# Optimization experiments

Hardware: AMD Instinct MI355X
Metric: run time of the kernel (lower is better)

## Reference

```python
import jax, jax.numpy as jnp
import numpy as np

B, T, C, NH = 8, 1024, 768, 12
HD = C // NH


def setup_inputs() -> dict:
    key = jax.random.key(0)
    k1, k2, k3, k4, k5 = jax.random.split(key, 5)
    s = 0.02
    return {
        "x": jax.random.normal(k1, (B, T, C), dtype=jnp.float32),
        "w_attn": jax.random.normal(k2, (C, 3 * C), dtype=jnp.float32) * s,
        "b_attn": jax.random.normal(k3, (3 * C,), dtype=jnp.float32) * s,
        "w_proj": jax.random.normal(k4, (C, C), dtype=jnp.float32) * s,
        "b_proj": jax.random.normal(k5, (C,), dtype=jnp.float32) * s,
    }


def reference(x, w_attn, b_attn, w_proj, b_proj):
    Bv, Tv, Cv = x.shape
    # fused QKV projection
    qkv = jnp.einsum('btc,cd->btd', x, w_attn) + b_attn  # [B,T,3C]
    q, k, v = jnp.split(qkv, 3, axis=-1)
    # [B, NH, T, HD]
    q = q.reshape(Bv, Tv, NH, HD).transpose(0, 2, 1, 3)
    k = k.reshape(Bv, Tv, NH, HD).transpose(0, 2, 1, 3)
    v = v.reshape(Bv, Tv, NH, HD).transpose(0, 2, 1, 3)
    scale = 1.0 / np.sqrt(HD).astype(np.float32)
    att = jnp.einsum('bhqd,bhkd->bhqk', q, k) * scale  # [B,NH,T,T]
    causal = jnp.tril(jnp.ones((Tv, Tv), dtype=bool))
    att = jnp.where(causal, att, -jnp.inf)
    att = jax.nn.softmax(att, axis=-1)
    y = jnp.einsum('bhqk,bhkd->bhqd', att, v)  # [B,NH,T,HD]
    y = y.transpose(0, 2, 1, 3).reshape(Bv, Tv, Cv)
    return jnp.einsum('btc,cd->btd', y, w_proj) + b_proj
```

## Files before the change

kernel.cpp:

```cpp
#include <hip/hip_runtime.h>

constexpr int kB  = 8;
constexpr int kT  = 1024;
constexpr int kC  = 768;
constexpr int kNH = 12;
constexpr int kHD = 64;
constexpr int kM  = kB * kT;
constexpr int k3C = 3 * kC;

using bf16x8 = __attribute__((ext_vector_type(8))) __bf16;
using f32x4  = __attribute__((ext_vector_type(4))) float;

__device__ __forceinline__ float bf2f(unsigned short u) {
    union { unsigned int i; float f; } v;
    v.i = ((unsigned int)u) << 16;
    return v.f;
}

__device__ __forceinline__ unsigned short f2bf(float f) {
    union { float f; unsigned int u; } v; v.f = f;
    unsigned int r = v.u + 0x7fffu + ((v.u >> 16) & 1u);
    return (unsigned short)(r >> 16);
}

__device__ __forceinline__ void async16(const void* g, void* l) {
    __builtin_amdgcn_global_load_lds(
        (__attribute__((address_space(1))) void*)g,
        (__attribute__((address_space(3))) void*)l, 16, 0, 0);
}

__device__ __forceinline__ void wait_vm0() {
    __builtin_amdgcn_s_waitcnt(0x0F70);
}


__global__ __launch_bounds__(256) void cvt_bf16_kernel(
    const float* __restrict__ in, unsigned short* __restrict__ out)
{
    const int i = blockIdx.x * 256 + threadIdx.x;
    const float4 v = ((const float4*)in)[i];
    ushort4 o;
    o.x = f2bf(v.x); o.y = f2bf(v.y); o.z = f2bf(v.z); o.w = f2bf(v.w);
    ((ushort4*)out)[i] = o;
}

__global__ __launch_bounds__(256) void transpose_cvt_kernel(
    const float* __restrict__ W, unsigned short* __restrict__ Wt, int K, int N)
{
    __shared__ float tile[32][33];
    const int tx = threadIdx.x & 31, ty = threadIdx.x >> 5;
    const int n0 = blockIdx.x * 32, k0 = blockIdx.y * 32;
    #pragma unroll
    for (int i = 0; i < 4; ++i)
        tile[ty + i * 8][tx] = W[(size_t)(k0 + ty + i * 8) * N + n0 + tx];
    __syncthreads();
    #pragma unroll
    for (int i = 0; i < 4; ++i)
        Wt[(size_t)(n0 + ty + i * 8) * K + k0 + tx] = f2bf(tile[tx][ty + i * 8]);
}

__global__ __launch_bounds__(256) void vtrans_kernel(
    const unsigned short* __restrict__ qkv, unsigned short* __restrict__ VT)
{
    __shared__ unsigned short tile[64][72];
    const int tid = threadIdx.x;
    const int bh = blockIdx.x >> 4;
    const int b = bh / kNH, h = bh % kNH;
    const int tt = (blockIdx.x & 15) * 64;
    const int row = tid >> 2;
    const int c0  = (tid & 3) * 16;
    const unsigned short* src =
        qkv + (size_t)(b * kT + tt + row) * k3C + 2 * kC + h * kHD + c0;
    *(uint4*)&tile[row][c0]     = *(const uint4*)src;
    *(uint4*)&tile[row][c0 + 8] = *(const uint4*)(src + 8);
    __syncthreads();
    const int d  = tid >> 2;
    const int t8 = (tid & 3) * 16;
    unsigned short tmp[16];
    #pragma unroll
    for (int i = 0; i < 16; ++i) tmp[i] = tile[t8 + i][d];
    unsigned short* dst = VT + ((size_t)bh * kHD + d) * kT + tt + t8;
    *(uint4*)dst       = *(uint4*)&tmp[0];
    *(uint4*)(dst + 8) = *(uint4*)&tmp[8];
}

template<bool OUT_BF16>
__global__ __launch_bounds__(256) void gemm_mfma_kernel(
    const unsigned short* __restrict__ A, int lda,
    const unsigned short* __restrict__ Bt,
    const float* __restrict__ bias,
    void* __restrict__ outv, int N, int K)
{
    alignas(16) __shared__ unsigned short As[16 * 512];
    alignas(16) __shared__ unsigned short Bs[16 * 512];

    const int tid  = threadIdx.x;
    const int w    = tid >> 6;
    const int lane = tid & 63;
    const int wr = w >> 1, wc = w & 1;
    const int m0 = blockIdx.y * 128, n0 = blockIdx.x * 128;

    const int fr = lane & 15;
    const int fk = (lane >> 4) * 8;

    f32x4 acc[4][4];
    #pragma unroll
    for (int i = 0; i < 4; ++i)
        #pragma unroll
        for (int j = 0; j < 4; ++j) {
            f32x4 z = {0.f, 0.f, 0.f, 0.f};
            acc[i][j] = z;
        }

    for (int kt = 0; kt < K; kt += 64) {
        #pragma unroll
        for (int t = 0; t < 4; ++t) {
            const int fa = w * 4 + t;
            const int ki = fa >> 3, si = fa & 7;
            const unsigned short* ga =
                A + (size_t)(m0 + si * 16 + fr) * lda + kt + ki * 32 + fk;
            async16(ga, &As[fa * 512]);
            const unsigned short* gb =
                Bt + (size_t)(n0 + si * 16 + fr) * K + kt + ki * 32 + fk;
            async16(gb, &Bs[fa * 512]);
        }
        wait_vm0();
        __syncthreads();

        #pragma unroll
        for (int ki = 0; ki < 2; ++ki) {
            bf16x8 a[4], b[4];
            #pragma unroll
            for (int i = 0; i < 4; ++i)
                a[i] = *(const bf16x8*)&As[(ki * 8 + wr * 4 + i) * 512 + lane * 8];
            #pragma unroll
            for (int j = 0; j < 4; ++j)
                b[j] = *(const bf16x8*)&Bs[(ki * 8 + wc * 4 + j) * 512 + lane * 8];
            #pragma unroll
            for (int i = 0; i < 4; ++i)
                #pragma unroll
                for (int j = 0; j < 4; ++j)
                    acc[i][j] = __builtin_amdgcn_mfma_f32_16x16x32_bf16(
                        a[i], b[j], acc[i][j], 0, 0, 0);
        }
        __syncthreads();
    }

    const int quad  = lane >> 4;
    const int col16 = lane & 15;
    float biasv[4];
    #pragma unroll
    for (int j = 0; j < 4; ++j)
        biasv[j] = bias[n0 + wc * 64 + j * 16 + col16];

    #pragma unroll
    for (int i = 0; i < 4; ++i) {
        #pragma unroll
        for (int r = 0; r < 4; ++r) {
            const int row = m0 + wr * 64 + i * 16 + quad * 4 + r;
            #pragma unroll
            for (int j = 0; j < 4; ++j) {
                const int col = n0 + wc * 64 + j * 16 + col16;
                const float v = acc[i][j][r] + biasv[j];
                if (OUT_BF16)
                    ((unsigned short*)outv)[(size_t)row * N + col] = f2bf(v);
                else
                    ((float*)outv)[(size_t)row * N + col] = v;
            }
        }
    }
}

__global__ __launch_bounds__(256) void attn_mfma_kernel(
    const unsigned short* __restrict__ qkv,
    const unsigned short* __restrict__ VT,
    unsigned short* __restrict__ y)
{
    alignas(16) __shared__ unsigned short Kf[2][8 * 512];
    alignas(16) __shared__ unsigned short Vf[2][8 * 512];
    alignas(16) __shared__ unsigned short Pf[8 * 512];

    const int tid  = threadIdx.x;
    const int w    = tid >> 6;
    const int lane = tid & 63;
    const int quad = lane >> 4, l15 = lane & 15;
    const int bh  = blockIdx.x >> 3;
    const int b   = bh / kNH, h = bh % kNH;
    const int pid = blockIdx.x & 7;

    auto stage = [&](int bufi, int kbase) {
        const unsigned short* gk = qkv +
            (size_t)(b * kT + kbase + w * 16 + l15) * k3C + kC + h * kHD + quad * 8;
        async16(gk,      &Kf[bufi][(w * 2 + 0) * 512]);
        async16(gk + 32, &Kf[bufi][(w * 2 + 1) * 512]);
        const unsigned short* gv = VT +
            ((size_t)bh * kHD + w * 16 + l15) * kT + kbase + quad * 8;
        async16(gv,      &Vf[bufi][(w * 2 + 0) * 512]);
        async16(gv + 32, &Vf[bufi][(w * 2 + 1) * 512]);
    };

    #pragma unroll 1
    for (int phase = 0; phase < 2; ++phase) {
        const int t0 = (phase == 0 ? (15 - pid) : pid) * 64;
        const int nchunks = t0 / 64 + 1;

        __syncthreads();
        stage(0, 0);
        {
            const unsigned short* g0 = qkv +
                (size_t)(b * kT + t0 + w * 16 + l15) * k3C + h * kHD + quad * 8;
            async16(g0,      &Pf[(w * 2 + 0) * 512]);
            async16(g0 + 32, &Pf[(w * 2 + 1) * 512]);
        }
        wait_vm0();
        const bf16x8 aq0 = *(const bf16x8*)&Pf[(w * 2 + 0) * 512 + lane * 8];
        const bf16x8 aq1 = *(const bf16x8*)&Pf[(w * 2 + 1) * 512 + lane * 8];

        float m_run[4], l_run[4];
        f32x4 acc_o[4];
        #pragma unroll
        for (int r = 0; r < 4; ++r) { m_run[r] = -INFINITY; l_run[r] = 0.f; }
        #pragma unroll
        for (int n = 0; n < 4; ++n) {
            f32x4 z = {0.f, 0.f, 0.f, 0.f};
            acc_o[n] = z;
        }

        for (int c = 0; c < nchunks; ++c) {
            const int kbase = c * 64;
            const int buf = c & 1;
            wait_vm0();
            __syncthreads();
            if (c + 1 < nchunks) stage(1 - buf, kbase + 64);

            f32x4 acc_s[4];
            #pragma unroll
            for (int k = 0; k < 4; ++k) {
                f32x4 z = {0.f, 0.f, 0.f, 0.f};
                acc_s[k] = z;
            }
            #pragma unroll
            for (int ksub = 0; ksub < 4; ++ksub) {
                const bf16x8 bk0 =
                    *(const bf16x8*)&Kf[buf][(ksub * 2 + 0) * 512 + lane * 8];
                const bf16x8 bk1 =
                    *(const bf16x8*)&Kf[buf][(ksub * 2 + 1) * 512 + lane * 8];
                acc_s[ksub] = __builtin_amdgcn_mfma_f32_16x16x32_bf16(
                    aq0, bk0, acc_s[ksub], 0, 0, 0);
                acc_s[ksub] = __builtin_amdgcn_mfma_f32_16x16x32_bf16(
                    aq1, bk1, acc_s[ksub], 0, 0, 0);
            }

            float sv[4][4];
            #pragma unroll
            for (int ksub = 0; ksub < 4; ++ksub)
                #pragma unroll
                for (int r = 0; r < 4; ++r)
                    sv[ksub][r] = acc_s[ksub][r] * 0.125f;
            if (kbase == t0) {
                const int qrow = t0 + w * 16 + quad * 4;
                #pragma unroll
                for (int ksub = 0; ksub < 4; ++ksub) {
                    const int key = kbase + ksub * 16 + l15;
                    #pragma unroll
                    for (int r = 0; r < 4; ++r)
                        if (key > qrow + r) sv[ksub][r] = -INFINITY;
                }
            }

            float alpha[4];
            #pragma unroll
            for (int r = 0; r < 4; ++r) {
                float mx = fmaxf(fmaxf(sv[0][r], sv[1][r]),
                                 fmaxf(sv[2][r], sv[3][r]));
                mx = fmaxf(mx, __shfl_xor(mx, 1));
                mx = fmaxf(mx, __shfl_xor(mx, 2));
                mx = fmaxf(mx, __shfl_xor(mx, 4));
                mx = fmaxf(mx, __shfl_xor(mx, 8));
                const float m_new = fmaxf(m_run[r], mx);
                alpha[r] = __expf(m_run[r] - m_new);
                float ps = 0.f;
                #pragma unroll
                for (int ksub = 0; ksub < 4; ++ksub) {
                    sv[ksub][r] = __expf(sv[ksub][r] - m_new);
                    ps += sv[ksub][r];
                }
                ps += __shfl_xor(ps, 1);
                ps += __shfl_xor(ps, 2);
                ps += __shfl_xor(ps, 4);
                ps += __shfl_xor(ps, 8);
                l_run[r] = l_run[r] * alpha[r] + ps;
                m_run[r] = m_new;
            }

            #pragma unroll
            for (int ksub = 0; ksub < 4; ++ksub) {
                const int key = ksub * 16 + l15;
                #pragma unroll
                for (int r = 0; r < 4; ++r) {
                    const int lp = quad * 4 + r + ((key & 31) >> 3) * 16;
                    Pf[(w * 2 + (key >> 5)) * 512 + lp * 8 + (key & 7)] =
                        f2bf(sv[ksub][r]);
                }
            }

            #pragma unroll
            for (int n = 0; n < 4; ++n)
                #pragma unroll
                for (int r = 0; r < 4; ++r)
                    acc_o[n][r] *= alpha[r];
            const bf16x8 ap0 = *(const bf16x8*)&Pf[(w * 2 + 0) * 512 + lane * 8];
            const bf16x8 ap1 = *(const bf16x8*)&Pf[(w * 2 + 1) * 512 + lane * 8];
            #pragma unroll
            for (int nsub = 0; nsub < 4; ++nsub) {
                const bf16x8 bv0 =
                    *(const bf16x8*)&Vf[buf][(nsub * 2 + 0) * 512 + lane * 8];
                const bf16x8 bv1 =
                    *(const bf16x8*)&Vf[buf][(nsub * 2 + 1) * 512 + lane * 8];
                acc_o[nsub] = __builtin_amdgcn_mfma_f32_16x16x32_bf16(
                    ap0, bv0, acc_o[nsub], 0, 0, 0);
                acc_o[nsub] = __builtin_amdgcn_mfma_f32_16x16x32_bf16(
                    ap1, bv1, acc_o[nsub], 0, 0, 0);
            }
        }

        float inv[4];
        #pragma unroll
        for (int r = 0; r < 4; ++r) inv[r] = 1.0f / l_run[r];
        #pragma unroll
        for (int nsub = 0; nsub < 4; ++nsub)
            #pragma unroll
            for (int r = 0; r < 4; ++r)
                y[(size_t)(b * kT + t0 + w * 16 + quad * 4 + r) * kC +
                  h * kHD + nsub * 16 + l15] = f2bf(acc_o[nsub][r] * inv[r]);
    }
}

extern "C" void kernel_launch(void* const* d_in, const int* in_sizes, int n_in,
                              void* d_out, int out_size, void* d_ws, size_t ws_size,
                              hipStream_t stream) {
    const float* x      = (const float*)d_in[0];
    const float* w_attn = (const float*)d_in[1];
    const float* b_attn = (const float*)d_in[2];
    const float* w_proj = (const float*)d_in[3];
    const float* b_proj = (const float*)d_in[4];
    float* out = (float*)d_out;

    unsigned short* xb     = (unsigned short*)d_ws;
    unsigned short* VT     = xb;
    unsigned short* wattnT = xb     + (size_t)kM * kC;
    unsigned short* wprojT = wattnT + (size_t)k3C * kC;
    unsigned short* qkv    = wprojT + (size_t)kC * kC;
    unsigned short* yb     = qkv    + (size_t)kM * k3C;

    cvt_bf16_kernel<<<(kM * kC) / (4 * 256), 256, 0, stream>>>(x, xb);
    transpose_cvt_kernel<<<dim3(k3C / 32, kC / 32), 256, 0, stream>>>(
        w_attn, wattnT, kC, k3C);
    transpose_cvt_kernel<<<dim3(kC / 32, kC / 32), 256, 0, stream>>>(
        w_proj, wprojT, kC, kC);

    gemm_mfma_kernel<true><<<dim3(k3C / 128, kM / 128), 256, 0, stream>>>(
        xb, kC, wattnT, b_attn, qkv, k3C, kC);

    vtrans_kernel<<<kB * kNH * (kT / 64), 256, 0, stream>>>(qkv, VT);

    attn_mfma_kernel<<<kB * kNH * 8, 256, 0, stream>>>(qkv, VT, yb);

    gemm_mfma_kernel<false><<<dim3(kC / 128, kM / 128), 256, 0, stream>>>(
        yb, kC, wprojT, b_proj, out, kC, kC);
}
```

Measured before the change: 249.3 us.

## Double-buffer GEMM k-tiles and use narrower N tiles for output projection

The MFMA GEMM now double-buffers its LDS tiles. The async global loads for the next 32-wide k-slice are issued while the current slice is being computed, which leaves one barrier per iteration instead of two. The N tile width becomes a template parameter, and the output projection GEMM uses 64-wide N tiles so it launches twice as many blocks on a small 768-wide output. The cost is a smaller k step per iteration and therefore more loop iterations and barriers per unit of work.

```diff
diff --git a/kernel.cpp b/kernel.cpp
--- a/kernel.cpp
+++ b/kernel.cpp
@@ -84,74 +84,82 @@
     *(uint4*)(dst + 8) = *(uint4*)&tmp[8];
 }
 
-template<bool OUT_BF16>
+template<int NSUB, bool OUT_BF16>
 __global__ __launch_bounds__(256) void gemm_mfma_kernel(
     const unsigned short* __restrict__ A, int lda,
     const unsigned short* __restrict__ Bt,
     const float* __restrict__ bias,
     void* __restrict__ outv, int N, int K)
 {
-    alignas(16) __shared__ unsigned short As[16 * 512];
-    alignas(16) __shared__ unsigned short Bs[16 * 512];
+    constexpr int NW = NSUB / 2;
+    constexpr int BB = NSUB / 4;
+    alignas(16) __shared__ unsigned short As[2][8 * 512];
+    alignas(16) __shared__ unsigned short Bs[2][NSUB * 512];
 
     const int tid  = threadIdx.x;
     const int w    = tid >> 6;
     const int lane = tid & 63;
     const int wr = w >> 1, wc = w & 1;
-    const int m0 = blockIdx.y * 128, n0 = blockIdx.x * 128;
+    const int m0 = blockIdx.y * 128, n0 = blockIdx.x * (NSUB * 16);
 
     const int fr = lane & 15;
     const int fk = (lane >> 4) * 8;
 
-    f32x4 acc[4][4];
+    auto stage = [&](int bufi, int kt) {
+        #pragma unroll
+        for (int t = 0; t < 2; ++t) {
+            const int fa = w * 2 + t;
+            const unsigned short* ga =
+                A + (size_t)(m0 + fa * 16 + fr) * lda + kt + fk;
+            async16(ga, &As[bufi][fa * 512]);
+        }
+        #pragma unroll
+        for (int t = 0; t < BB; ++t) {
+            const int fb = w * BB + t;
+            const unsigned short* gb =
+                Bt + (size_t)(n0 + fb * 16 + fr) * K + kt + fk;
+            async16(gb, &Bs[bufi][fb * 512]);
+        }
+    };
+
+    f32x4 acc[4][NW];
     #pragma unroll
     for (int i = 0; i < 4; ++i)
         #pragma unroll
-        for (int j = 0; j < 4; ++j) {
+        for (int j = 0; j < NW; ++j) {
             f32x4 z = {0.f, 0.f, 0.f, 0.f};
             acc[i][j] = z;
         }
 
-    for (int kt = 0; kt < K; kt += 64) {
-        #pragma unroll
-        for (int t = 0; t < 4; ++t) {
-            const int fa = w * 4 + t;
-            const int ki = fa >> 3, si = fa & 7;
-            const unsigned short* ga =
-                A + (size_t)(m0 + si * 16 + fr) * lda + kt + ki * 32 + fk;
-            async16(ga, &As[fa * 512]);
-            const unsigned short* gb =
-                Bt + (size_t)(n0 + si * 16 + fr) * K + kt + ki * 32 + fk;
-            async16(gb, &Bs[fa * 512]);
-        }
+    stage(0, 0);
+    const int niter = K / 32;
+    for (int it = 0; it < niter; ++it) {
+        const int buf = it & 1;
         wait_vm0();
         __syncthreads();
-
-        #pragma unroll
-        for (int ki = 0; ki < 2; ++ki) {
-            bf16x8 a[4], b[4];
-            #pragma unroll
-            for (int i = 0; i < 4; ++i)
-                a[i] = *(const bf16x8*)&As[(ki * 8 + wr * 4 + i) * 512 + lane * 8];
-            #pragma unroll
-            for (int j = 0; j < 4; ++j)
-                b[j] = *(const bf16x8*)&Bs[(ki * 8 + wc * 4 + j) * 512 + lane * 8];
-            #pragma unroll
-            for (int i = 0; i < 4; ++i)
-                #pragma unroll
-                for (int j = 0; j < 4; ++j)
-                    acc[i][j] = __builtin_amdgcn_mfma_f32_16x16x32_bf16(
-                        a[i], b[j], acc[i][j], 0, 0, 0);
-        }
-        __syncthreads();
+        if (it + 1 < niter) stage(1 - buf, (it + 1) * 32);
+
+        bf16x8 a[4], b[NW];
+        #pragma unroll
+        for (int i = 0; i < 4; ++i)
+            a[i] = *(const bf16x8*)&As[buf][(wr * 4 + i) * 512 + lane * 8];
+        #pragma unroll
+        for (int j = 0; j < NW; ++j)
+            b[j] = *(const bf16x8*)&Bs[buf][(wc * NW + j) * 512 + lane * 8];
+        #pragma unroll
+        for (int i = 0; i < 4; ++i)
+            #pragma unroll
+            for (int j = 0; j < NW; ++j)
+                acc[i][j] = __builtin_amdgcn_mfma_f32_16x16x32_bf16(
+                    a[i], b[j], acc[i][j], 0, 0, 0);
     }
 
     const int quad  = lane >> 4;
     const int col16 = lane & 15;
-    float biasv[4];
-    #pragma unroll
-    for (int j = 0; j < 4; ++j)
-        biasv[j] = bias[n0 + wc * 64 + j * 16 + col16];
+    float biasv[NW];
+    #pragma unroll
+    for (int j = 0; j < NW; ++j)
+        biasv[j] = bias[n0 + wc * (NW * 16) + j * 16 + col16];
 
     #pragma unroll
     for (int i = 0; i < 4; ++i) {
@@ -159,8 +167,8 @@
         for (int r = 0; r < 4; ++r) {
             const int row = m0 + wr * 64 + i * 16 + quad * 4 + r;
             #pragma unroll
-            for (int j = 0; j < 4; ++j) {
-                const int col = n0 + wc * 64 + j * 16 + col16;
+            for (int j = 0; j < NW; ++j) {
+                const int col = n0 + wc * (NW * 16) + j * 16 + col16;
                 const float v = acc[i][j][r] + biasv[j];
                 if (OUT_BF16)
                     ((unsigned short*)outv)[(size_t)row * N + col] = f2bf(v);
@@ -359,13 +367,13 @@
     transpose_cvt_kernel<<<dim3(kC / 32, kC / 32), 256, 0, stream>>>(
         w_proj, wprojT, kC, kC);
 
-    gemm_mfma_kernel<true><<<dim3(k3C / 128, kM / 128), 256, 0, stream>>>(
+    gemm_mfma_kernel<8, true><<<dim3(k3C / 128, kM / 128), 256, 0, stream>>>(
         xb, kC, wattnT, b_attn, qkv, k3C, kC);
 
     vtrans_kernel<<<kB * kNH * (kT / 64), 256, 0, stream>>>(qkv, VT);
 
     attn_mfma_kernel<<<kB * kNH * 8, 256, 0, stream>>>(qkv, VT, yb);
 
-    gemm_mfma_kernel<false><<<dim3(kC / 128, kM / 128), 256, 0, stream>>>(
+    gemm_mfma_kernel<4, false><<<dim3(kC / 64, kM / 128), 256, 0, stream>>>(
         yb, kC, wprojT, b_proj, out, kC, kC);
 }
```

Measured after the change: 242.8 us. 1.03x faster.
